# Optimization experiments

Measured on AMD Instinct MI355X. Metric: run time of the kernel, lower is better.

## Reference

```python
import jax, jax.numpy as jnp
import numpy as np

B, C, H, W = 2, 3, 96, 96
D = 32  # qkv channels

def setup_inputs() -> dict:
    key = jax.random.key(0)
    ks = jax.random.split(key, 9)
    s3 = 1.0 / np.sqrt(3.0)
    sD = 1.0 / np.sqrt(float(D))
    return {
        "image": jax.random.normal(ks[0], (B, C, H, W), dtype=jnp.float32),
        "key_w": jax.random.normal(ks[1], (D, C), dtype=jnp.float32) * s3,
        "key_b": jax.random.normal(ks[2], (D,), dtype=jnp.float32) * 0.01,
        "query_w": jax.random.normal(ks[3], (D, C), dtype=jnp.float32) * s3,
        "query_b": jax.random.normal(ks[4], (D,), dtype=jnp.float32) * 0.01,
        "value_w": jax.random.normal(ks[5], (D, C), dtype=jnp.float32) * s3,
        "value_b": jax.random.normal(ks[6], (D,), dtype=jnp.float32) * 0.01,
        "out_w": jax.random.normal(ks[7], (C, D), dtype=jnp.float32) * sD,
        "out_b": jax.random.normal(ks[8], (C,), dtype=jnp.float32) * 0.01,
    }

def reference(image, key_w, key_b, query_w, query_b, value_w, value_b, out_w, out_b):
    b, c, h, w = image.shape
    n = h * w
    x = image.reshape(b, c, n)  # [B,3,N]
    # 1x1 convs == per-pixel linear maps over channels
    f_x = jnp.einsum('dc,bcn->bdn', key_w, x) + key_b[None, :, None]    # key   [B,D,N]
    g_x = jnp.einsum('dc,bcn->bdn', query_w, x) + query_b[None, :, None]  # query [B,D,N]
    h_x = jnp.einsum('dc,bcn->bdn', value_w, x) + value_b[None, :, None]  # value [B,D,N]
    # s = f_x^T @ g_x : [B,N,N]; softmax over dim=1 (first N axis), as in torch code
    s = jnp.einsum('bdn,bdm->bnm', f_x, g_x)
    beta = jax.nn.softmax(s, axis=1)
    # v = h_x @ beta : [B,D,N]
    v = jnp.einsum('bdn,bnm->bdm', h_x, beta)
    # output 1x1 conv D->3, then clamp
    o = jnp.einsum('cd,bdm->bcm', out_w, v) + out_b[None, :, None]
    o = jnp.clip(o, -1.0, 1.0)
    return o.reshape(b, c, h, w)
```

## Files before the change

kernel.cpp:

```cpp
#include <hip/hip_runtime.h>
#include <hip/hip_fp16.h>

#define BB 2
#define CC 3
#define NN 9216
#define DD 32
#define NSPLIT 8
#define KSPLIT 2
#define KEYS_PER_WAVE (NN / (KSPLIT * NSPLIT))
#define CHUNKS (KEYS_PER_WAVE / 64)
#define NGROUP (BB * NN / 32)
#define L2E 1.44269504f

typedef _Float16 half8 __attribute__((ext_vector_type(8)));
typedef _Float16 half4v __attribute__((ext_vector_type(4)));
typedef __fp16 fp16x2 __attribute__((ext_vector_type(2)));
typedef float float4v __attribute__((ext_vector_type(4)));

#define MFMA_K32(a, b, c) __builtin_amdgcn_mfma_f32_16x16x32_f16((a), (b), (c), 0, 0, 0)

__global__ __launch_bounds__(256) void prep_kernel(
    const float* __restrict__ img,
    const float* __restrict__ kw, const float* __restrict__ kb,
    const float* __restrict__ qw, const float* __restrict__ qb,
    const float* __restrict__ vw, const float* __restrict__ vb,
    const float* __restrict__ ow,
    _Float16* __restrict__ fH, _Float16* __restrict__ fL,
    _Float16* __restrict__ gH, _Float16* __restrict__ gL,
    _Float16* __restrict__ hP)
{
    __shared__ float cwb[12];
    int bid = blockIdx.x;
    if (bid < 288) {
        int id = bid * 256 + threadIdx.x;
        int part = id & 3;
        int n = (id >> 2) % NN;
        int b = (id >> 2) / NN;
        const float* xb = img + (size_t)b * CC * NN + n;
        float x0 = xb[0], x1 = xb[NN], x2 = xb[2 * NN];
        half8 fh, fl, gh, gl;
#pragma unroll
        for (int j = 0; j < 8; j++) {
            int d = part * 8 + j;
            float fv = kw[d * 3 + 0] * x0 + kw[d * 3 + 1] * x1 + kw[d * 3 + 2] * x2 + kb[d];
            float gv = (qw[d * 3 + 0] * x0 + qw[d * 3 + 1] * x1 + qw[d * 3 + 2] * x2 + qb[d]) * L2E;
            _Float16 fhi = (_Float16)fv;
            _Float16 ghi = (_Float16)gv;
            fh[j] = fhi; fl[j] = (_Float16)(fv - (float)fhi);
            gh[j] = ghi; gl[j] = (_Float16)(gv - (float)ghi);
        }
        size_t off = ((size_t)b * NN + n) * DD + part * 8;
        *(half8*)(fH + off) = fh;
        *(half8*)(fL + off) = fl;
        *(half8*)(gH + off) = gh;
        *(half8*)(gL + off) = gl;
    } else {
        int t = threadIdx.x;
        if (t < 9) {
            int c = t / 3, k = t % 3;
            float s = 0.f;
#pragma unroll
            for (int d = 0; d < DD; d++) s += ow[c * DD + d] * vw[d * 3 + k];
            cwb[t] = s;
        } else if (t < 12) {
            int c = t - 9;
            float s = 0.f;
#pragma unroll
            for (int d = 0; d < DD; d++) s += ow[c * DD + d] * vb[d];
            cwb[9 + c] = s;
        }
        __syncthreads();
        const int N8 = NN / 8;
        int id = (bid - 288) * 256 + t;
        int n8 = id % N8;
        int row = (id / N8) & 3;
        int b = id / (N8 * 4);
        half8 hv = {0, 0, 0, 0, 0, 0, 0, 0};
        if (row < 3) {
            const float* xb = img + (size_t)b * CC * NN + n8 * 8;
            float w0 = cwb[row * 3 + 0], w1 = cwb[row * 3 + 1],
                  w2 = cwb[row * 3 + 2], bv = cwb[9 + row];
#pragma unroll
            for (int j = 0; j < 8; j++)
                hv[j] = (_Float16)(w0 * xb[j] + w1 * xb[NN + j] + w2 * xb[2 * NN + j] + bv);
        }
        *(half8*)(hP + ((size_t)(b * 4 + row)) * NN + n8 * 8) = hv;
    }
}

__global__ __launch_bounds__(512, 4) void attn_partial_kernel(
    const _Float16* __restrict__ fH, const _Float16* __restrict__ fL,
    const _Float16* __restrict__ gH, const _Float16* __restrict__ gL,
    const _Float16* __restrict__ hP,
    float* __restrict__ pnum, float* __restrict__ pM, float* __restrict__ pL)
{
    const int gb = blockIdx.x;
    const int g  = gb >> 1;
    const int ks = gb & 1;
    const int b = g / (NN / 32);
    const int m0 = (g % (NN / 32)) * 32;
    const int tid = threadIdx.x;
    const int w = tid >> 6;
    const int lane = tid & 63;
    const int l16 = lane & 15;
    const int quad = lane >> 4;

    union SMem {
        _Float16 P[NSPLIT * 2 * 16 * 72];
        float acc[NSPLIT][CC][33];
    };
    __shared__ __align__(16) SMem sm;
    __shared__ float mbuf[NSPLIT][32];
    __shared__ float lbuf[NSPLIT][4][32];

    const _Float16* gHb = gH + ((size_t)b * NN + m0 + l16) * DD + quad * 8;
    const _Float16* gLb = gL + ((size_t)b * NN + m0 + l16) * DD + quad * 8;
    half8 qh0 = *(const half8*)(gHb);
    half8 ql0 = *(const half8*)(gLb);
    half8 qh1 = *(const half8*)(gHb + (size_t)16 * DD);
    half8 ql1 = *(const half8*)(gLb + (size_t)16 * DD);

    float4v acc0 = {0,0,0,0};
    float4v acc1 = {0,0,0,0};
    float mrun0 = -1e30f, lrun0 = 0.f;
    float mrun1 = -1e30f, lrun1 = 0.f;

    const int nbase = ks * (NN / KSPLIT) + w * KEYS_PER_WAVE;
    const int vrow = (l16 < 3) ? l16 : 3;
    const _Float16* vp = hP + ((size_t)(b * 4 + vrow)) * NN + nbase + quad * 8;
    const _Float16* khp = fH + ((size_t)b * NN + nbase + l16) * DD + quad * 8;
    const _Float16* klp = fL + ((size_t)b * NN + nbase + l16) * DD + quad * 8;
    _Float16* Pw0 = sm.P + (size_t)(w * 2 + 0) * 16 * 72;
    _Float16* Pw1 = sm.P + (size_t)(w * 2 + 1) * 16 * 72;

    for (int c = 0; c < CHUNKS; ++c) {
        half8 ka[4], kl[4];
#pragma unroll
        for (int blk = 0; blk < 4; blk++) {
            ka[blk] = *(const half8*)(khp + (size_t)(c * 64 + blk * 16) * DD);
            kl[blk] = *(const half8*)(klp + (size_t)(c * 64 + blk * 16) * DD);
        }
        half8 vA0 = *(const half8*)(vp + c * 64);
        half8 vA1 = *(const half8*)(vp + c * 64 + 32);

        {
            float4v s[4];
#pragma unroll
            for (int blk = 0; blk < 4; blk++) {
                float4v z = {0,0,0,0};
                float4v t = MFMA_K32(ka[blk], ql0, z);
                t = MFMA_K32(kl[blk], qh0, t);
                s[blk] = MFMA_K32(ka[blk], qh0, t);
            }
            float mb0 = fmaxf(fmaxf(s[0][0], s[0][1]), fmaxf(s[0][2], s[0][3]));
            float mb1 = fmaxf(fmaxf(s[1][0], s[1][1]), fmaxf(s[1][2], s[1][3]));
            float mb2 = fmaxf(fmaxf(s[2][0], s[2][1]), fmaxf(s[2][2], s[2][3]));
            float mb3 = fmaxf(fmaxf(s[3][0], s[3][1]), fmaxf(s[3][2], s[3][3]));
            float mx = fmaxf(fmaxf(mb0, mb1), fmaxf(mb2, mb3));
            mx = fmaxf(mx, __shfl_xor(mx, 16, 64));
            mx = fmaxf(mx, __shfl_xor(mx, 32, 64));
            float mnew = fmaxf(mrun0, mx);
            float rsum = 0.f;
#pragma unroll
            for (int blk = 0; blk < 4; blk++) {
                float p0 = __builtin_amdgcn_exp2f(s[blk][0] - mnew);
                float p1 = __builtin_amdgcn_exp2f(s[blk][1] - mnew);
                float p2 = __builtin_amdgcn_exp2f(s[blk][2] - mnew);
                float p3 = __builtin_amdgcn_exp2f(s[blk][3] - mnew);
                union { fp16x2 h2[2]; half4v h4; } u;
                u.h2[0] = __builtin_amdgcn_cvt_pkrtz(p0, p1);
                u.h2[1] = __builtin_amdgcn_cvt_pkrtz(p2, p3);
                *(half4v*)(Pw0 + l16 * 72 + blk * 16 + quad * 4) = u.h4;
                rsum += (p0 + p1) + (p2 + p3);
            }
            if (__any(mnew > mrun0)) {
                float alpha = __builtin_amdgcn_exp2f(mrun0 - mnew);
#pragma unroll
                for (int r = 0; r < 4; r++) acc0[r] *= alpha;
                lrun0 = lrun0 * alpha + rsum;
                mrun0 = mnew;
            } else {
                lrun0 += rsum;
            }
        }
        {
            float4v s[4];
#pragma unroll
            for (int blk = 0; blk < 4; blk++) {
                float4v z = {0,0,0,0};
                float4v t = MFMA_K32(ka[blk], ql1, z);
                t = MFMA_K32(kl[blk], qh1, t);
                s[blk] = MFMA_K32(ka[blk], qh1, t);
            }
            float mb0 = fmaxf(fmaxf(s[0][0], s[0][1]), fmaxf(s[0][2], s[0][3]));
            float mb1 = fmaxf(fmaxf(s[1][0], s[1][1]), fmaxf(s[1][2], s[1][3]));
            float mb2 = fmaxf(fmaxf(s[2][0], s[2][1]), fmaxf(s[2][2], s[2][3]));
            float mb3 = fmaxf(fmaxf(s[3][0], s[3][1]), fmaxf(s[3][2], s[3][3]));
            float mx = fmaxf(fmaxf(mb0, mb1), fmaxf(mb2, mb3));
            mx = fmaxf(mx, __shfl_xor(mx, 16, 64));
            mx = fmaxf(mx, __shfl_xor(mx, 32, 64));
            float mnew = fmaxf(mrun1, mx);
            float rsum = 0.f;
#pragma unroll
            for (int blk = 0; blk < 4; blk++) {
                float p0 = __builtin_amdgcn_exp2f(s[blk][0] - mnew);
                float p1 = __builtin_amdgcn_exp2f(s[blk][1] - mnew);
                float p2 = __builtin_amdgcn_exp2f(s[blk][2] - mnew);
                float p3 = __builtin_amdgcn_exp2f(s[blk][3] - mnew);
                union { fp16x2 h2[2]; half4v h4; } u;
                u.h2[0] = __builtin_amdgcn_cvt_pkrtz(p0, p1);
                u.h2[1] = __builtin_amdgcn_cvt_pkrtz(p2, p3);
                *(half4v*)(Pw1 + l16 * 72 + blk * 16 + quad * 4) = u.h4;
                rsum += (p0 + p1) + (p2 + p3);
            }
            if (__any(mnew > mrun1)) {
                float alpha = __builtin_amdgcn_exp2f(mrun1 - mnew);
#pragma unroll
                for (int r = 0; r < 4; r++) acc1[r] *= alpha;
                lrun1 = lrun1 * alpha + rsum;
                mrun1 = mnew;
            } else {
                lrun1 += rsum;
            }
        }
        {
            half8 pf0 = *(const half8*)(Pw0 + l16 * 72 + quad * 8);
            half8 pf1 = *(const half8*)(Pw0 + l16 * 72 + 32 + quad * 8);
            acc0 = MFMA_K32(vA0, pf0, acc0);
            acc0 = MFMA_K32(vA1, pf1, acc0);
            half8 qf0 = *(const half8*)(Pw1 + l16 * 72 + quad * 8);
            half8 qf1 = *(const half8*)(Pw1 + l16 * 72 + 32 + quad * 8);
            acc1 = MFMA_K32(vA0, qf0, acc1);
            acc1 = MFMA_K32(vA1, qf1, acc1);
        }
    }

    __syncthreads();

    mbuf[w][l16]            = mrun0;
    mbuf[w][l16 + 16]       = mrun1;
    lbuf[w][quad][l16]      = lrun0;
    lbuf[w][quad][l16 + 16] = lrun1;
    if (quad == 0) {
#pragma unroll
        for (int r = 0; r < 3; r++) {
            sm.acc[w][r][l16]      = acc0[r];
            sm.acc[w][r][l16 + 16] = acc1[r];
        }
    }
    __syncthreads();

    if (tid < CC * 32) {
        int c = tid >> 5, m = tid & 31;
        float M = mbuf[0][m];
#pragma unroll
        for (int s2 = 1; s2 < NSPLIT; s2++) M = fmaxf(M, mbuf[s2][m]);
        float L = 0.f, num = 0.f;
#pragma unroll
        for (int s2 = 0; s2 < NSPLIT; s2++) {
            float e2 = __builtin_amdgcn_exp2f(mbuf[s2][m] - M);
            float lsum = (lbuf[s2][0][m] + lbuf[s2][1][m]) + (lbuf[s2][2][m] + lbuf[s2][3][m]);
            L += lsum * e2;
            num += sm.acc[s2][c][m] * e2;
        }
        pnum[(size_t)gb * (CC * 32) + tid] = num;
        if (c == 0) { pM[gb * 32 + m] = M; pL[gb * 32 + m] = L; }
    }
}

__global__ __launch_bounds__(128) void merge_kernel(
    const float* __restrict__ pnum, const float* __restrict__ pM,
    const float* __restrict__ pL, const float* __restrict__ ob,
    float* __restrict__ out)
{
    const int g = blockIdx.x;
    const int b = g / (NN / 32);
    const int m0 = (g % (NN / 32)) * 32;
    const int tid = threadIdx.x;
    const int gb0 = g * 2, gb1 = g * 2 + 1;

    if (tid < CC * 32) {
        int c = tid >> 5, m = tid & 31;
        float M0 = pM[gb0 * 32 + m], M1 = pM[gb1 * 32 + m];
        float M = fmaxf(M0, M1);
        float e0 = __builtin_amdgcn_exp2f(M0 - M);
        float e1 = __builtin_amdgcn_exp2f(M1 - M);
        float L = pL[gb0 * 32 + m] * e0 + pL[gb1 * 32 + m] * e1;
        float num = pnum[(size_t)gb0 * (CC * 32) + tid] * e0 +
                    pnum[(size_t)gb1 * (CC * 32) + tid] * e1;
        float o = num / L + ob[c];
        o = fminf(1.f, fmaxf(-1.f, o));
        out[((size_t)b * CC + c) * NN + m0 + m] = o;
    }
}

extern "C" void kernel_launch(void* const* d_in, const int* in_sizes, int n_in,
                              void* d_out, int out_size, void* d_ws, size_t ws_size,
                              hipStream_t stream) {
    const float* img = (const float*)d_in[0];
    const float* kw  = (const float*)d_in[1];
    const float* kb  = (const float*)d_in[2];
    const float* qw  = (const float*)d_in[3];
    const float* qb  = (const float*)d_in[4];
    const float* vw  = (const float*)d_in[5];
    const float* vb  = (const float*)d_in[6];
    const float* ow  = (const float*)d_in[7];
    const float* ob  = (const float*)d_in[8];
    float* out = (float*)d_out;

    const size_t sz = (size_t)BB * NN * DD;
    _Float16* fH = (_Float16*)d_ws;
    _Float16* fL = fH + sz;
    _Float16* gH = fL + sz;
    _Float16* gL = gH + sz;
    _Float16* hP = gL + sz;
    float* pnum = (float*)(hP + (size_t)BB * 4 * NN);
    float* pM   = pnum + (size_t)NGROUP * KSPLIT * CC * 32;
    float* pL   = pM + (size_t)NGROUP * KSPLIT * 32;

    prep_kernel<<<324, 256, 0, stream>>>(img, kw, kb, qw, qb, vw, vb, ow,
                                         fH, fL, gH, gL, hP);
    attn_partial_kernel<<<NGROUP * KSPLIT, 512, 0, stream>>>(
        fH, fL, gH, gL, hP, pnum, pM, pL);
    merge_kernel<<<NGROUP, 128, 0, stream>>>(pnum, pM, pL, ob, out);
}
```

Baseline: 135.5 us.

## Feed softmax probabilities to PV MFMA directly from registers, dropping LDS round-trip

The exponentiated scores, laid out as the S MFMA output, are now used directly as the B operand of 16x16x16 MFMAs. The value fragments are reloaded in a matching half4 layout, one per 16-key block. This removes the per-chunk LDS store and reload of P, and shrinks shared memory to the small accumulator and statistic buffers. The launch-bounds occupancy hint goes from 4 to 6 blocks, which may force register spilling, and the PV product now takes twice as many smaller MFMA instructions.

```diff
diff --git a/kernel.cpp b/kernel.cpp
--- a/kernel.cpp
+++ b/kernel.cpp
@@ -18,6 +18,7 @@
 typedef float float4v __attribute__((ext_vector_type(4)));
 
 #define MFMA_K32(a, b, c) __builtin_amdgcn_mfma_f32_16x16x32_f16((a), (b), (c), 0, 0, 0)
+#define MFMA_K16(a, b, c) __builtin_amdgcn_mfma_f32_16x16x16f16((a), (b), (c), 0, 0, 0)
 
 __global__ __launch_bounds__(256) void prep_kernel(
     const float* __restrict__ img,
@@ -88,7 +89,7 @@
     }
 }
 
-__global__ __launch_bounds__(512, 4) void attn_partial_kernel(
+__global__ __launch_bounds__(512, 6) void attn_partial_kernel(
     const _Float16* __restrict__ fH, const _Float16* __restrict__ fL,
     const _Float16* __restrict__ gH, const _Float16* __restrict__ gL,
     const _Float16* __restrict__ hP,
@@ -105,11 +106,7 @@
     const int l16 = lane & 15;
     const int quad = lane >> 4;
 
-    union SMem {
-        _Float16 P[NSPLIT * 2 * 16 * 72];
-        float acc[NSPLIT][CC][33];
-    };
-    __shared__ __align__(16) SMem sm;
+    __shared__ float accbuf[NSPLIT][CC][33];
     __shared__ float mbuf[NSPLIT][32];
     __shared__ float lbuf[NSPLIT][4][32];
 
@@ -127,21 +124,19 @@
 
     const int nbase = ks * (NN / KSPLIT) + w * KEYS_PER_WAVE;
     const int vrow = (l16 < 3) ? l16 : 3;
-    const _Float16* vp = hP + ((size_t)(b * 4 + vrow)) * NN + nbase + quad * 8;
+    const _Float16* vp = hP + ((size_t)(b * 4 + vrow)) * NN + nbase + quad * 4;
     const _Float16* khp = fH + ((size_t)b * NN + nbase + l16) * DD + quad * 8;
     const _Float16* klp = fL + ((size_t)b * NN + nbase + l16) * DD + quad * 8;
-    _Float16* Pw0 = sm.P + (size_t)(w * 2 + 0) * 16 * 72;
-    _Float16* Pw1 = sm.P + (size_t)(w * 2 + 1) * 16 * 72;
 
     for (int c = 0; c < CHUNKS; ++c) {
         half8 ka[4], kl[4];
+        half4v vA[4];
 #pragma unroll
         for (int blk = 0; blk < 4; blk++) {
             ka[blk] = *(const half8*)(khp + (size_t)(c * 64 + blk * 16) * DD);
             kl[blk] = *(const half8*)(klp + (size_t)(c * 64 + blk * 16) * DD);
-        }
-        half8 vA0 = *(const half8*)(vp + c * 64);
-        half8 vA1 = *(const half8*)(vp + c * 64 + 32);
+            vA[blk] = *(const half4v*)(vp + c * 64 + blk * 16);
+        }
 
         {
             float4v s[4];
@@ -161,6 +156,7 @@
             mx = fmaxf(mx, __shfl_xor(mx, 32, 64));
             float mnew = fmaxf(mrun0, mx);
             float rsum = 0.f;
+            half4v pv[4];
 #pragma unroll
             for (int blk = 0; blk < 4; blk++) {
                 float p0 = __builtin_amdgcn_exp2f(s[blk][0] - mnew);
@@ -170,7 +166,7 @@
                 union { fp16x2 h2[2]; half4v h4; } u;
                 u.h2[0] = __builtin_amdgcn_cvt_pkrtz(p0, p1);
                 u.h2[1] = __builtin_amdgcn_cvt_pkrtz(p2, p3);
-                *(half4v*)(Pw0 + l16 * 72 + blk * 16 + quad * 4) = u.h4;
+                pv[blk] = u.h4;
                 rsum += (p0 + p1) + (p2 + p3);
             }
             if (__any(mnew > mrun0)) {
@@ -182,6 +178,9 @@
             } else {
                 lrun0 += rsum;
             }
+#pragma unroll
+            for (int blk = 0; blk < 4; blk++)
+                acc0 = MFMA_K16(vA[blk], pv[blk], acc0);
         }
         {
             float4v s[4];
@@ -201,6 +200,7 @@
             mx = fmaxf(mx, __shfl_xor(mx, 32, 64));
             float mnew = fmaxf(mrun1, mx);
             float rsum = 0.f;
+            half4v pv[4];
 #pragma unroll
             for (int blk = 0; blk < 4; blk++) {
                 float p0 = __builtin_amdgcn_exp2f(s[blk][0] - mnew);
@@ -210,7 +210,7 @@
                 union { fp16x2 h2[2]; half4v h4; } u;
                 u.h2[0] = __builtin_amdgcn_cvt_pkrtz(p0, p1);
                 u.h2[1] = __builtin_amdgcn_cvt_pkrtz(p2, p3);
-                *(half4v*)(Pw1 + l16 * 72 + blk * 16 + quad * 4) = u.h4;
+                pv[blk] = u.h4;
                 rsum += (p0 + p1) + (p2 + p3);
             }
             if (__any(mnew > mrun1)) {
@@ -222,20 +222,11 @@
             } else {
                 lrun1 += rsum;
             }
-        }
-        {
-            half8 pf0 = *(const half8*)(Pw0 + l16 * 72 + quad * 8);
-            half8 pf1 = *(const half8*)(Pw0 + l16 * 72 + 32 + quad * 8);
-            acc0 = MFMA_K32(vA0, pf0, acc0);
-            acc0 = MFMA_K32(vA1, pf1, acc0);
-            half8 qf0 = *(const half8*)(Pw1 + l16 * 72 + quad * 8);
-            half8 qf1 = *(const half8*)(Pw1 + l16 * 72 + 32 + quad * 8);
-            acc1 = MFMA_K32(vA0, qf0, acc1);
-            acc1 = MFMA_K32(vA1, qf1, acc1);
-        }
-    }
-
-    __syncthreads();
+#pragma unroll
+            for (int blk = 0; blk < 4; blk++)
+                acc1 = MFMA_K16(vA[blk], pv[blk], acc1);
+        }
+    }
 
     mbuf[w][l16]            = mrun0;
     mbuf[w][l16 + 16]       = mrun1;
@@ -244,8 +235,8 @@
     if (quad == 0) {
 #pragma unroll
         for (int r = 0; r < 3; r++) {
-            sm.acc[w][r][l16]      = acc0[r];
-            sm.acc[w][r][l16 + 16] = acc1[r];
+            accbuf[w][r][l16]      = acc0[r];
+            accbuf[w][r][l16 + 16] = acc1[r];
         }
     }
     __syncthreads();
@@ -261,7 +252,7 @@
             float e2 = __builtin_amdgcn_exp2f(mbuf[s2][m] - M);
             float lsum = (lbuf[s2][0][m] + lbuf[s2][1][m]) + (lbuf[s2][2][m] + lbuf[s2][3][m]);
             L += lsum * e2;
-            num += sm.acc[s2][c][m] * e2;
+            num += accbuf[s2][c][m] * e2;
         }
         pnum[(size_t)gb * (CC * 32) + tid] = num;
         if (c == 0) { pM[gb * 32 + m] = M; pL[gb * 32 + m] = L; }
```

Result: slower. 199.6 us (+47.3%).
